# Optimization experiments

Hardware: AMD Instinct MI355X
Metric: run time of the kernel (lower is better)

Reference implementation:

```python
import jax, jax.numpy as jnp
import numpy as np

PATCH = 7
PAD = PATCH // 2  # 3


def _to_gray(x):
    # x: [B,3,H,W] -> [B,1,H,W]
    return 0.299 * x[:, 0:1] + 0.587 * x[:, 1:2] + 0.114 * x[:, 2:3]


def _census_transform(x):
    # x: [B,C,H,W] RGB -> grayscale, then 48 shifted binary comparisons.
    if x.shape[1] == 3:
        x = _to_gray(x)
    B, C, H, W = x.shape
    x_pad = jnp.pad(x, ((0, 0), (0, 0), (PAD, PAD), (PAD, PAD)), mode='reflect')
    center = x
    feats = []
    for i in range(PATCH):
        for j in range(PATCH):
            if i == PAD and j == PAD:
                continue
            neighbor = x_pad[:, :, i:i + H, j:j + W]
            feats.append((center > neighbor).astype(x.dtype))
    return jnp.concatenate(feats, axis=1)  # [B,48,H,W]


def setup_inputs() -> dict:
    key = jax.random.key(0)
    k1, k2 = jax.random.split(key)
    B, C, H, W = 8, 3, 512, 512
    pred = jax.random.uniform(k1, (B, C, H, W), dtype=jnp.float32)
    target = jax.random.uniform(k2, (B, C, H, W), dtype=jnp.float32)
    return {"pred": pred, "target": target}


def reference(pred, target):
    pred_census = _census_transform(pred)
    target_census = _census_transform(target)
    return jnp.abs(pred_census - target_census).mean()
```

## Files before the change

### kernel.cpp

```cpp
#include <hip/hip_runtime.h>


#define BATCH 8
#define HH 512
#define WW 512
#define PLANE (HH * WW)
#define TW 64
#define TH 32
#define SCOLS 72
#define HROWS 38
#define KPR 18
#define PITCH 44
#define NT 512
#define LDSZ (SCOLS * PITCH)

__device__ __forceinline__ int refl(int v, int n) {
    return v < 0 ? -v : (v >= n ? 2 * n - 2 - v : v);
}
__device__ __forceinline__ int cbase(int lx) {
    return lx * PITCH + (((lx >> 2) & 7) << 2);
}

__device__ __forceinline__ void load_col10(const float* col, float (&w)[10]) {
    const float4 a = *(const float4*)(col);
    const float4 b = *(const float4*)(col + 4);
    const float2 d = *(const float2*)(col + 8);
    w[0] = a.x; w[1] = a.y; w[2] = a.z; w[3] = a.w;
    w[4] = b.x; w[5] = b.y; w[6] = b.z; w[7] = b.w;
    w[8] = d.x; w[9] = d.y;
}

__global__ __launch_bounds__(NT, 8)
void census_fused(const float* __restrict__ pred,
                  const float* __restrict__ target,
                  float* __restrict__ out) {
    __shared__ __align__(16) float sP[LDSZ];
    __shared__ __align__(16) float sT[LDSZ];

    const int b   = blockIdx.z;
    const int ty0 = blockIdx.y * TH;
    const int tx0 = blockIdx.x * TW;
    const float* __restrict__ pb = pred   + (size_t)b * 3 * PLANE;
    const float* __restrict__ tb = target + (size_t)b * 3 * PLANE;
    const bool fastx = (blockIdx.x >= 1 && blockIdx.x <= 6);

    if (fastx) {
        for (int idx = threadIdx.x; idx < HROWS * KPR; idx += NT) {
            const int hy = idx / KPR;
            const int k  = idx - hy * KPR;
            const int gy  = refl(ty0 + hy - 3, HH);
            const int off = gy * WW + tx0 - 4 + 4 * k;
            const float4 pr = *(const float4*)(pb + off);
            const float4 pg = *(const float4*)(pb + off + PLANE);
            const float4 pc = *(const float4*)(pb + off + 2 * PLANE);
            const float4 tr = *(const float4*)(tb + off);
            const float4 tg = *(const float4*)(tb + off + PLANE);
            const float4 tc = *(const float4*)(tb + off + 2 * PLANE);
            const int lx = 4 * k;
            sP[cbase(lx + 0) + hy] = 0.299f * pr.x + 0.587f * pg.x + 0.114f * pc.x;
            sP[cbase(lx + 1) + hy] = 0.299f * pr.y + 0.587f * pg.y + 0.114f * pc.y;
            sP[cbase(lx + 2) + hy] = 0.299f * pr.z + 0.587f * pg.z + 0.114f * pc.z;
            sP[cbase(lx + 3) + hy] = 0.299f * pr.w + 0.587f * pg.w + 0.114f * pc.w;
            sT[cbase(lx + 0) + hy] = 0.299f * tr.x + 0.587f * tg.x + 0.114f * tc.x;
            sT[cbase(lx + 1) + hy] = 0.299f * tr.y + 0.587f * tg.y + 0.114f * tc.y;
            sT[cbase(lx + 2) + hy] = 0.299f * tr.z + 0.587f * tg.z + 0.114f * tc.z;
            sT[cbase(lx + 3) + hy] = 0.299f * tr.w + 0.587f * tg.w + 0.114f * tc.w;
        }
    } else {
        for (int idx = threadIdx.x; idx < HROWS * SCOLS; idx += NT) {
            const int hy = idx / SCOLS;
            const int lx = idx - hy * SCOLS;
            const int gy  = refl(ty0 + hy - 3, HH);
            const int gx  = refl(tx0 + lx - 4, WW);
            const int off = gy * WW + gx;
            sP[cbase(lx) + hy] = 0.299f * pb[off] + 0.587f * pb[off + PLANE] + 0.114f * pb[off + 2 * PLANE];
            sT[cbase(lx) + hy] = 0.299f * tb[off] + 0.587f * tb[off + PLANE] + 0.114f * tb[off + 2 * PLANE];
        }
    }
    __syncthreads();

    const int wv  = threadIdx.x >> 6;
    const int c   = threadIdx.x & 63;
    const int pr0 = wv * 4;

    float wP[10], wT[10], cP[4], cT[4];
    int cnt = 0;
    load_col10(&sP[cbase(c + 4) + pr0], wP);
    load_col10(&sT[cbase(c + 4) + pr0], wT);
    #pragma unroll
    for (int p = 0; p < 4; ++p) { cP[p] = wP[3 + p]; cT[p] = wT[3 + p]; }
    #pragma unroll
    for (int p = 0; p < 4; ++p) {
        #pragma unroll
        for (int dy = -3; dy <= 3; ++dy) {
            if (dy == 0) continue;
            cnt += ((cP[p] > wP[3 + p + dy]) != (cT[p] > wT[3 + p + dy])) ? 1 : 0;
        }
    }
    #pragma unroll
    for (int t = 0; t < 6; ++t) {
        const int lx = c + 1 + (t < 3 ? t : t + 1);
        load_col10(&sP[cbase(lx) + pr0], wP);
        load_col10(&sT[cbase(lx) + pr0], wT);
        #pragma unroll
        for (int p = 0; p < 4; ++p) {
            #pragma unroll
            for (int dy = -3; dy <= 3; ++dy)
                cnt += ((cP[p] > wP[3 + p + dy]) != (cT[p] > wT[3 + p + dy])) ? 1 : 0;
        }
    }

    #pragma unroll
    for (int o = 32; o > 0; o >>= 1) cnt += __shfl_down(cnt, o, 64);
    __shared__ int wsum[8];
    if ((threadIdx.x & 63) == 0) wsum[wv] = cnt;
    __syncthreads();
    if (threadIdx.x == 0) {
        int tot = 0;
        #pragma unroll
        for (int w = 0; w < 8; ++w) tot += wsum[w];
        atomicAdd(out, (float)tot * (1.0f / 100663296.0f));
    }
}

extern "C" void kernel_launch(void* const* d_in, const int* in_sizes, int n_in,
                              void* d_out, int out_size, void* d_ws, size_t ws_size,
                              hipStream_t stream) {
    const float* pred   = (const float*)d_in[0];
    const float* target = (const float*)d_in[1];
    float* out = (float*)d_out;

    hipMemsetAsync(out, 0, sizeof(float), stream);

    dim3 grid(WW / TW, HH / TH, BATCH);
    census_fused<<<grid, NT, 0, stream>>>(pred, target, out);
}
```

Before: 98.55 us.

## Double tile height and overlap second-band staging with first-band compute

```diff
diff --git a/kernel.cpp b/kernel.cpp
--- a/kernel.cpp
+++ b/kernel.cpp
@@ -6,13 +6,15 @@
 #define WW 512
 #define PLANE (HH * WW)
 #define TW 64
-#define TH 32
+#define TH 64
 #define SCOLS 72
-#define HROWS 38
+#define HROWS 70
+#define AROWS 38
+#define BROWS 32
 #define KPR 18
-#define PITCH 44
+#define PITCH 72
 #define NT 512
-#define LDSZ (SCOLS * PITCH)
+#define LDSZ (SCOLS * PITCH + 8)
 
 __device__ __forceinline__ int refl(int v, int n) {
     return v < 0 ? -v : (v >= n ? 2 * n - 2 - v : v);
@@ -30,7 +32,7 @@
     w[8] = d.x; w[9] = d.y;
 }
 
-__global__ __launch_bounds__(NT, 8)
+__global__ __launch_bounds__(NT, 4)
 void census_fused(const float* __restrict__ pred,
                   const float* __restrict__ target,
                   float* __restrict__ out) {
@@ -44,71 +46,95 @@
     const float* __restrict__ tb = target + (size_t)b * 3 * PLANE;
     const bool fastx = (blockIdx.x >= 1 && blockIdx.x <= 6);
 
+    auto stage_f4 = [&](int hy, int k) {
+        const int gy  = refl(ty0 + hy - 3, HH);
+        const int off = gy * WW + tx0 - 4 + 4 * k;
+        const float4 pr = *(const float4*)(pb + off);
+        const float4 pg = *(const float4*)(pb + off + PLANE);
+        const float4 pc = *(const float4*)(pb + off + 2 * PLANE);
+        const float4 tr = *(const float4*)(tb + off);
+        const float4 tg = *(const float4*)(tb + off + PLANE);
+        const float4 tc = *(const float4*)(tb + off + 2 * PLANE);
+        const int lx = 4 * k;
+        sP[cbase(lx + 0) + hy] = 0.299f * pr.x + 0.587f * pg.x + 0.114f * pc.x;
+        sP[cbase(lx + 1) + hy] = 0.299f * pr.y + 0.587f * pg.y + 0.114f * pc.y;
+        sP[cbase(lx + 2) + hy] = 0.299f * pr.z + 0.587f * pg.z + 0.114f * pc.z;
+        sP[cbase(lx + 3) + hy] = 0.299f * pr.w + 0.587f * pg.w + 0.114f * pc.w;
+        sT[cbase(lx + 0) + hy] = 0.299f * tr.x + 0.587f * tg.x + 0.114f * tc.x;
+        sT[cbase(lx + 1) + hy] = 0.299f * tr.y + 0.587f * tg.y + 0.114f * tc.y;
+        sT[cbase(lx + 2) + hy] = 0.299f * tr.z + 0.587f * tg.z + 0.114f * tc.z;
+        sT[cbase(lx + 3) + hy] = 0.299f * tr.w + 0.587f * tg.w + 0.114f * tc.w;
+    };
+    auto stage_sc = [&](int hy, int lx) {
+        const int gy  = refl(ty0 + hy - 3, HH);
+        const int gx  = refl(tx0 + lx - 4, WW);
+        const int off = gy * WW + gx;
+        sP[cbase(lx) + hy] = 0.299f * pb[off] + 0.587f * pb[off + PLANE] + 0.114f * pb[off + 2 * PLANE];
+        sT[cbase(lx) + hy] = 0.299f * tb[off] + 0.587f * tb[off + PLANE] + 0.114f * tb[off + 2 * PLANE];
+    };
+
     if (fastx) {
-        for (int idx = threadIdx.x; idx < HROWS * KPR; idx += NT) {
+        for (int idx = threadIdx.x; idx < AROWS * KPR; idx += NT) {
             const int hy = idx / KPR;
-            const int k  = idx - hy * KPR;
-            const int gy  = refl(ty0 + hy - 3, HH);
-            const int off = gy * WW + tx0 - 4 + 4 * k;
-            const float4 pr = *(const float4*)(pb + off);
-            const float4 pg = *(const float4*)(pb + off + PLANE);
-            const float4 pc = *(const float4*)(pb + off + 2 * PLANE);
-            const float4 tr = *(const float4*)(tb + off);
-            const float4 tg = *(const float4*)(tb + off + PLANE);
-            const float4 tc = *(const float4*)(tb + off + 2 * PLANE);
-            const int lx = 4 * k;
-            sP[cbase(lx + 0) + hy] = 0.299f * pr.x + 0.587f * pg.x + 0.114f * pc.x;
-            sP[cbase(lx + 1) + hy] = 0.299f * pr.y + 0.587f * pg.y + 0.114f * pc.y;
-            sP[cbase(lx + 2) + hy] = 0.299f * pr.z + 0.587f * pg.z + 0.114f * pc.z;
-            sP[cbase(lx + 3) + hy] = 0.299f * pr.w + 0.587f * pg.w + 0.114f * pc.w;
-            sT[cbase(lx + 0) + hy] = 0.299f * tr.x + 0.587f * tg.x + 0.114f * tc.x;
-            sT[cbase(lx + 1) + hy] = 0.299f * tr.y + 0.587f * tg.y + 0.114f * tc.y;
-            sT[cbase(lx + 2) + hy] = 0.299f * tr.z + 0.587f * tg.z + 0.114f * tc.z;
-            sT[cbase(lx + 3) + hy] = 0.299f * tr.w + 0.587f * tg.w + 0.114f * tc.w;
+            stage_f4(hy, idx - hy * KPR);
         }
     } else {
-        for (int idx = threadIdx.x; idx < HROWS * SCOLS; idx += NT) {
+        for (int idx = threadIdx.x; idx < AROWS * SCOLS; idx += NT) {
             const int hy = idx / SCOLS;
-            const int lx = idx - hy * SCOLS;
-            const int gy  = refl(ty0 + hy - 3, HH);
-            const int gx  = refl(tx0 + lx - 4, WW);
-            const int off = gy * WW + gx;
-            sP[cbase(lx) + hy] = 0.299f * pb[off] + 0.587f * pb[off + PLANE] + 0.114f * pb[off + 2 * PLANE];
-            sT[cbase(lx) + hy] = 0.299f * tb[off] + 0.587f * tb[off + PLANE] + 0.114f * tb[off + 2 * PLANE];
+            stage_sc(hy, idx - hy * SCOLS);
         }
     }
     __syncthreads();
+
+    if (fastx) {
+        for (int idx = threadIdx.x; idx < BROWS * KPR; idx += NT) {
+            const int hy = idx / KPR;
+            stage_f4(AROWS + hy, idx - hy * KPR);
+        }
+    } else {
+        for (int idx = threadIdx.x; idx < BROWS * SCOLS; idx += NT) {
+            const int hy = idx / SCOLS;
+            stage_sc(AROWS + hy, idx - hy * SCOLS);
+        }
+    }
 
     const int wv  = threadIdx.x >> 6;
     const int c   = threadIdx.x & 63;
     const int pr0 = wv * 4;
 
-    float wP[10], wT[10], cP[4], cT[4];
-    int cnt = 0;
-    load_col10(&sP[cbase(c + 4) + pr0], wP);
-    load_col10(&sT[cbase(c + 4) + pr0], wT);
-    #pragma unroll
-    for (int p = 0; p < 4; ++p) { cP[p] = wP[3 + p]; cT[p] = wT[3 + p]; }
-    #pragma unroll
-    for (int p = 0; p < 4; ++p) {
+    auto band_count = [&](int r0) -> int {
+        float wP[10], wT[10], cP[4], cT[4];
+        int cnt = 0;
+        load_col10(&sP[cbase(c + 4) + r0], wP);
+        load_col10(&sT[cbase(c + 4) + r0], wT);
         #pragma unroll
-        for (int dy = -3; dy <= 3; ++dy) {
-            if (dy == 0) continue;
-            cnt += ((cP[p] > wP[3 + p + dy]) != (cT[p] > wT[3 + p + dy])) ? 1 : 0;
-        }
-    }
-    #pragma unroll
-    for (int t = 0; t < 6; ++t) {
-        const int lx = c + 1 + (t < 3 ? t : t + 1);
-        load_col10(&sP[cbase(lx) + pr0], wP);
-        load_col10(&sT[cbase(lx) + pr0], wT);
+        for (int p = 0; p < 4; ++p) { cP[p] = wP[3 + p]; cT[p] = wT[3 + p]; }
         #pragma unroll
         for (int p = 0; p < 4; ++p) {
             #pragma unroll
-            for (int dy = -3; dy <= 3; ++dy)
+            for (int dy = -3; dy <= 3; ++dy) {
+                if (dy == 0) continue;
                 cnt += ((cP[p] > wP[3 + p + dy]) != (cT[p] > wT[3 + p + dy])) ? 1 : 0;
+            }
         }
-    }
+        #pragma unroll
+        for (int t = 0; t < 6; ++t) {
+            const int lx = c + 1 + (t < 3 ? t : t + 1);
+            load_col10(&sP[cbase(lx) + r0], wP);
+            load_col10(&sT[cbase(lx) + r0], wT);
+            #pragma unroll
+            for (int p = 0; p < 4; ++p) {
+                #pragma unroll
+                for (int dy = -3; dy <= 3; ++dy)
+                    cnt += ((cP[p] > wP[3 + p + dy]) != (cT[p] > wT[3 + p + dy])) ? 1 : 0;
+            }
+        }
+        return cnt;
+    };
+
+    int cnt = band_count(pr0);
+    __syncthreads();
+    cnt += band_count(32 + pr0);
 
     #pragma unroll
     for (int o = 32; o > 0; o >>= 1) cnt += __shfl_down(cnt, o, 64);
```

New measurement: 101.4 us. +2.8%, slower.

## Exploit census pair symmetry to halve comparisons with border correction

Applied to the files above, without the earlier changes.

```diff
diff --git a/kernel.cpp b/kernel.cpp
--- a/kernel.cpp
+++ b/kernel.cpp
@@ -26,6 +26,12 @@
     const float4 b = *(const float4*)(col + 4);
     const float2 d = *(const float2*)(col + 8);
     w[0] = a.x; w[1] = a.y; w[2] = a.z; w[3] = a.w;
+    w[4] = b.x; w[5] = b.y; w[6] = b.z; w[7] = b.w;
+    w[8] = d.x; w[9] = d.y;
+}
+__device__ __forceinline__ void load_col6hi(const float* col, float (&w)[10]) {
+    const float4 b = *(const float4*)(col + 4);
+    const float2 d = *(const float2*)(col + 8);
     w[4] = b.x; w[5] = b.y; w[6] = b.z; w[7] = b.w;
     w[8] = d.x; w[9] = d.y;
 }
@@ -92,21 +98,61 @@
     #pragma unroll
     for (int p = 0; p < 4; ++p) {
         #pragma unroll
-        for (int dy = -3; dy <= 3; ++dy) {
-            if (dy == 0) continue;
+        for (int dy = 1; dy <= 3; ++dy)
             cnt += ((cP[p] > wP[3 + p + dy]) != (cT[p] > wT[3 + p + dy])) ? 1 : 0;
+    }
+    #pragma unroll
+    for (int t = 0; t < 3; ++t) {
+        const int lx = c + 1 + t;
+        load_col6hi(&sP[cbase(lx) + pr0], wP);
+        load_col6hi(&sT[cbase(lx) + pr0], wT);
+        #pragma unroll
+        for (int p = 0; p < 4; ++p) {
+            #pragma unroll
+            for (int dy = 1; dy <= 3; ++dy)
+                cnt += ((cP[p] > wP[3 + p + dy]) != (cT[p] > wT[3 + p + dy])) ? 1 : 0;
         }
     }
     #pragma unroll
-    for (int t = 0; t < 6; ++t) {
-        const int lx = c + 1 + (t < 3 ? t : t + 1);
+    for (int t = 0; t < 3; ++t) {
+        const int lx = c + 5 + t;
         load_col10(&sP[cbase(lx) + pr0], wP);
         load_col10(&sT[cbase(lx) + pr0], wT);
         #pragma unroll
         for (int p = 0; p < 4; ++p) {
             #pragma unroll
-            for (int dy = -3; dy <= 3; ++dy)
+            for (int dy = 0; dy <= 3; ++dy)
                 cnt += ((cP[p] > wP[3 + p + dy]) != (cT[p] > wT[3 + p + dy])) ? 1 : 0;
+        }
+    }
+    cnt *= 2;
+
+    if (tx0 == 0 || tx0 + TW == WW || ty0 == 0 || ty0 + TH == HH) {
+        const int gx = tx0 + c;
+        #pragma unroll 1
+        for (int p = 0; p < 4; ++p) {
+            const int gy = ty0 + pr0 + p;
+            if (gx >= 3 && gx <= WW - 4 && gy >= 3 && gy <= HH - 4) continue;
+            const float cp = sP[cbase(c + 4) + pr0 + 3 + p];
+            const float ct = sT[cbase(c + 4) + pr0 + 3 + p];
+            #pragma unroll 1
+            for (int k = 0; k < 24; ++k) {
+                int dy, dx;
+                if (k < 3) { dy = 0; dx = k + 1; }
+                else { const int j = k - 3; dy = 1 + j / 7; dx = (j % 7) - 3; }
+                if ((unsigned)(gy - dy) > (unsigned)(HH - 1) ||
+                    (unsigned)(gx - dx) > (unsigned)(WW - 1)) {
+                    const float np = sP[cbase(c + 4 - dx) + pr0 + 3 + p - dy];
+                    const float nt = sT[cbase(c + 4 - dx) + pr0 + 3 + p - dy];
+                    cnt += ((cp > np) != (ct > nt)) ? 1 : 0;
+                }
+                if ((unsigned)(gy + dy) > (unsigned)(HH - 1) ||
+                    (unsigned)(gx + dx) > (unsigned)(WW - 1)) {
+                    const float np = sP[cbase(c + 4 + dx) + pr0 + 3 + p + dy];
+                    const float nt = sT[cbase(c + 4 + dx) + pr0 + 3 + p + dy];
+                    cnt -= ((cp > np) != (ct > nt)) ? 1 : 0;
+                }
+            }
         }
     }
 
```

After: 133.0 us. 1.35x slower.

## Exploit census comparison symmetry to halve comparisons, add border correction kernel

Applied to the files above, without the earlier changes.

```diff
diff --git a/kernel.cpp b/kernel.cpp
--- a/kernel.cpp
+++ b/kernel.cpp
@@ -13,6 +13,7 @@
 #define PITCH 44
 #define NT 512
 #define LDSZ (SCOLS * PITCH)
+#define NBORDER 6108
 
 __device__ __forceinline__ int refl(int v, int n) {
     return v < 0 ? -v : (v >= n ? 2 * n - 2 - v : v);
@@ -92,23 +93,34 @@
     #pragma unroll
     for (int p = 0; p < 4; ++p) {
         #pragma unroll
-        for (int dy = -3; dy <= 3; ++dy) {
-            if (dy == 0) continue;
+        for (int dy = 1; dy <= 3; ++dy)
             cnt += ((cP[p] > wP[3 + p + dy]) != (cT[p] > wT[3 + p + dy])) ? 1 : 0;
-        }
-    }
-    #pragma unroll
-    for (int t = 0; t < 6; ++t) {
-        const int lx = c + 1 + (t < 3 ? t : t + 1);
+    }
+    #pragma unroll
+    for (int t = 0; t < 3; ++t) {
+        const int lx = c + 1 + t;
         load_col10(&sP[cbase(lx) + pr0], wP);
         load_col10(&sT[cbase(lx) + pr0], wT);
         #pragma unroll
         for (int p = 0; p < 4; ++p) {
             #pragma unroll
-            for (int dy = -3; dy <= 3; ++dy)
+            for (int dy = 1; dy <= 3; ++dy)
                 cnt += ((cP[p] > wP[3 + p + dy]) != (cT[p] > wT[3 + p + dy])) ? 1 : 0;
         }
     }
+    #pragma unroll
+    for (int t = 0; t < 3; ++t) {
+        const int lx = c + 5 + t;
+        load_col10(&sP[cbase(lx) + pr0], wP);
+        load_col10(&sT[cbase(lx) + pr0], wT);
+        #pragma unroll
+        for (int p = 0; p < 4; ++p) {
+            #pragma unroll
+            for (int dy = 0; dy <= 3; ++dy)
+                cnt += ((cP[p] > wP[3 + p + dy]) != (cT[p] > wT[3 + p + dy])) ? 1 : 0;
+        }
+    }
+    cnt *= 2;
 
     #pragma unroll
     for (int o = 32; o > 0; o >>= 1) cnt += __shfl_down(cnt, o, 64);
@@ -123,6 +135,61 @@
     }
 }
 
+__global__ __launch_bounds__(256)
+void census_border(const float* __restrict__ pred,
+                   const float* __restrict__ target,
+                   float* __restrict__ out) {
+    const int b = blockIdx.y;
+    const float* __restrict__ pb = pred   + (size_t)b * 3 * PLANE;
+    const float* __restrict__ tb = target + (size_t)b * 3 * PLANE;
+    const int tid = blockIdx.x * 256 + threadIdx.x;
+    int cnt = 0;
+    if (tid < NBORDER) {
+        int x, y;
+        if (tid < 1536)      { y = tid >> 9; x = tid & 511; }
+        else if (tid < 3072) { const int t = tid - 1536; y = 509 + (t >> 9); x = t & 511; }
+        else if (tid < 4590) { const int t = tid - 3072; x = t / 506; y = 3 + (t - 506 * (t / 506)); }
+        else                 { const int t = tid - 4590; x = 509 + t / 506; y = 3 + (t - 506 * (t / 506)); }
+        auto gray = [&](const float* img, int xx, int yy) -> float {
+            const int o = yy * WW + xx;
+            return 0.299f * img[o] + 0.587f * img[o + PLANE] + 0.114f * img[o + 2 * PLANE];
+        };
+        const float cp = gray(pb, x, y), ct = gray(tb, x, y);
+        #pragma unroll
+        for (int dy = 0; dy <= 3; ++dy) {
+            #pragma unroll
+            for (int dx = -3; dx <= 3; ++dx) {
+                if (dy == 0 && dx <= 0) continue;
+                {
+                    const int xm = x - dx, ym = y - dy;
+                    if ((unsigned)xm >= WW || (unsigned)ym >= HH) {
+                        const int nx = refl(xm, WW), ny = refl(ym, HH);
+                        const float np = gray(pb, nx, ny), nt = gray(tb, nx, ny);
+                        cnt += ((cp > np) != (ct > nt)) ? 1 : 0;
+                    }
+                }
+                {
+                    const int xp = x + dx, yp = y + dy;
+                    if ((unsigned)xp >= WW || (unsigned)yp >= HH) {
+                        const int nx = refl(xp, WW), ny = refl(yp, HH);
+                        const float np = gray(pb, nx, ny), nt = gray(tb, nx, ny);
+                        cnt -= ((cp > np) != (ct > nt)) ? 1 : 0;
+                    }
+                }
+            }
+        }
+    }
+    #pragma unroll
+    for (int o = 32; o > 0; o >>= 1) cnt += __shfl_down(cnt, o, 64);
+    __shared__ int ws[4];
+    if ((threadIdx.x & 63) == 0) ws[threadIdx.x >> 6] = cnt;
+    __syncthreads();
+    if (threadIdx.x == 0) {
+        const int tot = ws[0] + ws[1] + ws[2] + ws[3];
+        atomicAdd(out, (float)tot * (1.0f / 100663296.0f));
+    }
+}
+
 extern "C" void kernel_launch(void* const* d_in, const int* in_sizes, int n_in,
                               void* d_out, int out_size, void* d_ws, size_t ws_size,
                               hipStream_t stream) {
@@ -134,4 +201,7 @@
 
     dim3 grid(WW / TW, HH / TH, BATCH);
     census_fused<<<grid, NT, 0, stream>>>(pred, target, out);
-}
+
+    dim3 gb((NBORDER + 255) / 256, BATCH);
+    census_border<<<gb, 256, 0, stream>>>(pred, target, out);
+}
```

After: 126.4 us. 1.28x slower.
